# Kernel tuning notes

Hardware: AMD Instinct MI355X
Metric: run time of the kernel (lower is better)

The kernel has to match this reference:

```python
import jax, jax.numpy as jnp
import numpy as np

SIGMA = 1.0
DELTA = 1.0
TOPK = 10
TOPK_HALF = 5  # int(np.around(TOPK / 2))


def l2norm(x):
    # F.normalize: x / max(||x||, 1e-12)
    n = jnp.linalg.norm(x, axis=-1, keepdims=True)
    return x / jnp.maximum(n, 1e-12)


def cdist(a, b):
    # pairwise euclidean distance with grad-safe sqrt (0 on exact-zero dists)
    d2 = (jnp.sum(a * a, axis=1)[:, None] + jnp.sum(b * b, axis=1)[None, :]
          - 2.0 * a @ b.T)
    d2 = jnp.maximum(d2, 0.0)
    return jnp.where(d2 > 0.0, jnp.sqrt(jnp.where(d2 > 0.0, d2, 1.0)), 0.0)


def rc_weights(t_emb, idx):
    # all of this is under torch.no_grad() in the original
    N = t_emb.shape[0]
    T_dist = cdist(t_emb, t_emb)
    W_P = jnp.exp(-(T_dist ** 2) / SIGMA)
    same_id = idx[:, None] == idx[None, :]
    W_P_copy = jnp.where(same_id, 1.0, W_P)
    _, topk_index = jax.lax.top_k(W_P_copy, TOPK)            # [N, k]
    topk_half_index = topk_index[:, :TOPK_HALF]               # [N, k/2]
    rows = jnp.arange(N)[:, None]
    W_NN = jnp.zeros((N, N), W_P.dtype).at[rows, topk_index].set(1.0)
    V = (((W_NN + W_NN.T) / 2.0) == 1.0).astype(W_P.dtype)    # mutual-NN graph
    # vectorized form of the per-row loop:
    # W_C_tilda[i, j] = V[i, j] * |N(i) \cap N(j)| / |N(i)|
    deg = V.sum(axis=1)                                       # |N(i)| per row
    VV = V @ V                                                # V symmetric -> (V@V)[i,j] = |N(i) cap N(j)|
    W_C_tilda = jnp.where(V > 0.0, VV / jnp.maximum(deg, 1.0)[:, None], 0.0)
    W_C_hat = W_C_tilda[topk_half_index].mean(axis=1)         # [N, N]
    W_C = (W_C_hat + W_C_hat.T) / 2.0
    W = (W_P + W_C) / 2.0
    off_diag = 1.0 - jnp.eye(N, dtype=W.dtype)
    pos_weight = W * off_diag
    neg_weight = (1.0 - W) * off_diag
    return pos_weight, neg_weight


def rc_loss(s_emb, t_emb, idx):
    s_emb = l2norm(s_emb)        # disable_mu=True
    t_emb = l2norm(t_emb)
    N = s_emb.shape[0]
    S_dist = cdist(s_emb, s_emb)
    S_dist = S_dist / S_dist.mean(axis=1, keepdims=True)
    pos_w, neg_w = rc_weights(t_emb, idx)
    pos_w = jax.lax.stop_gradient(pos_w)
    neg_w = jax.lax.stop_gradient(neg_w)
    pull = jax.nn.relu(S_dist) ** 2 * pos_w
    push = jax.nn.relu(DELTA - S_dist) ** 2 * neg_w
    return (pull.sum() + push.sum()) / (N * (N - 1))


def kl_loss(s_f, s_g):
    # disable_mu=True -> normalize both
    s_f = l2norm(s_f)
    s_g = l2norm(s_g)
    N = s_f.shape[0]
    S_dist = cdist(s_f, s_f)
    S_dist = S_dist / S_dist.mean(axis=1, keepdims=True)
    S_bg = cdist(s_g, s_g)
    S_bg = S_bg / S_bg.mean(axis=1, keepdims=True)
    log_q = jax.nn.log_softmax(-S_dist, axis=-1)
    log_p = jax.nn.log_softmax(jax.lax.stop_gradient(-S_bg), axis=-1)
    p = jnp.exp(log_p)
    return jnp.sum(p * (log_p - log_q)) / N


def setup_inputs() -> dict:
    key = jax.random.key(0)
    k1, k2, k3, k4 = jax.random.split(key, 4)
    N = 4096
    s_f = jax.random.normal(k1, (N, 512), jnp.float32)
    s_g = jax.random.normal(k2, (N, 512), jnp.float32)
    t_g = jax.random.normal(k3, (N, 1024), jnp.float32)
    idx = jax.random.randint(k4, (N,), 0, 2048, jnp.int64 if jax.config.jax_enable_x64 else jnp.int32)
    return {"s_f": s_f, "s_g": s_g, "t_g": t_g, "idx": idx}


def reference(s_f, s_g, t_g, idx):
    loss_RC_f = rc_loss(s_f, t_g, idx)
    loss_RC_g = rc_loss(s_g, t_g, idx)
    loss_RC = (loss_RC_f + loss_RC_g) / 2.0
    loss_KL = kl_loss(s_f, s_g)
    return loss_RC, loss_KL, loss_RC + loss_KL
```

## Files before the change

kernel.cpp:

```cpp
#include <hip/hip_runtime.h>
#include <hip/hip_bf16.h>

#define NN 4096
typedef unsigned short u16;
typedef __bf16 bf16x8 __attribute__((ext_vector_type(8)));
typedef float f32x4 __attribute__((ext_vector_type(4)));
typedef u16 u16x8 __attribute__((ext_vector_type(8)));

typedef const __attribute__((address_space(1))) void* gptr_t;
typedef __attribute__((address_space(3))) void* lptr_t;

__device__ inline u16 bf16bits(float v) {
    __bf16 h = (__bf16)v;
    return __builtin_bit_cast(u16, h);
}
__device__ inline float bf16val(float v) {
    __bf16 h = (__bf16)v;
    return (float)h;
}
__device__ inline float b2f(u16 b) { return __uint_as_float(((unsigned)b) << 16); }

__device__ inline float block_sum(float v, volatile float* sbuf) {
    int lane = threadIdx.x & 63, wv = threadIdx.x >> 6;
#pragma unroll
    for (int o = 32; o > 0; o >>= 1) v += __shfl_xor(v, o, 64);
    if (lane == 0) sbuf[wv] = v;
    __syncthreads();
    float r = sbuf[0] + sbuf[1] + sbuf[2] + sbuf[3];
    __syncthreads();
    return r;
}

template <int D>
__global__ void normalize_kernel(const float* __restrict__ in, u16* __restrict__ outb,
                                 float* __restrict__ ssout) {
    __shared__ float sbuf[4];
    constexpr int NV = D / 4;
    int row = blockIdx.x, tid = threadIdx.x;
    const float4* x4 = (const float4*)(in + (size_t)row * D);
    float4 v = make_float4(0.f, 0.f, 0.f, 0.f);
    if (tid < NV) v = x4[tid];
    float s = v.x * v.x + v.y * v.y + v.z * v.z + v.w * v.w;
    float tot = block_sum(s, sbuf);
    float inv = 1.0f / fmaxf(sqrtf(tot), 1e-12f);
    float sb = 0.f;
    if (tid < NV) {
        float b0 = bf16val(v.x * inv), b1 = bf16val(v.y * inv);
        float b2 = bf16val(v.z * inv), b3 = bf16val(v.w * inv);
        ushort4 o;
        o.x = bf16bits(v.x * inv);
        o.y = bf16bits(v.y * inv);
        o.z = bf16bits(v.z * inv);
        o.w = bf16bits(v.w * inv);
        ((ushort4*)(outb + (size_t)row * D))[tid] = o;
        sb = b0 * b0 + b1 * b1 + b2 * b2 + b3 * b3;
    }
    float totb = block_sum(sb, sbuf);
    if (tid == 0) ssout[row] = totb;
}

#define TS 132
__launch_bounds__(256)
__global__ void gram_merged(const u16* __restrict__ tb, const u16* __restrict__ fb,
                            const u16* __restrict__ gb, const float* __restrict__ ss_t,
                            const float* __restrict__ ss_f, const float* __restrict__ ss_g,
                            u16* __restrict__ WP, u16* __restrict__ Sf, u16* __restrict__ Sg) {
    __shared__ __align__(16) u16 smem[24576];

    int bid = blockIdx.x;
    int seg = (bid < 528) ? 0 : (bid < 1056 ? 1 : 2);
    int p = bid - seg * 528;
    int l = (p & 7) * 66 + (p >> 3);
    int by = 0, rem = l;
    while (rem >= 32 - by) { rem -= 32 - by; ++by; }
    int bx = by + rem;

    const u16* X = (seg == 0) ? tb : (seg == 1 ? fb : gb);
    const float* ss = (seg == 0) ? ss_t : (seg == 1 ? ss_f : ss_g);
    u16* outp = (seg == 0) ? WP : (seg == 1 ? Sf : Sg);
    const int K = (seg == 0) ? 1024 : 512;
    const bool mode1 = (seg != 0);
    const bool offdiag = (bx != by);

    const int tid = threadIdx.x;
    const int wv = tid >> 6, lane = tid & 63;
    const int wr = wv >> 1, wc = wv & 1;
    const int brow = by * 128, bcol = bx * 128;
    const int r = lane & 15, kc = lane >> 4;
    const int crow = lane >> 2;
    const int koff = (lane & 3) * 8;

    f32x4 acc[4][4];
#pragma unroll
    for (int mi = 0; mi < 4; ++mi)
#pragma unroll
        for (int ni = 0; ni < 4; ++ni) acc[mi][ni] = (f32x4){0.f, 0.f, 0.f, 0.f};

    auto STAGE = [&](int buf, int k0) {
#pragma unroll
        for (int cc = 0; cc < 2; ++cc) {
            int c = wv * 2 + cc;
            const u16* ga = X + (size_t)(brow + c * 16 + crow) * K + k0 + koff;
            const u16* gbp = X + (size_t)(bcol + c * 16 + crow) * K + k0 + koff;
            __builtin_amdgcn_global_load_lds((gptr_t)ga, (lptr_t)&smem[buf * 4096 + c * 512], 16, 0, 0);
            __builtin_amdgcn_global_load_lds((gptr_t)gbp, (lptr_t)&smem[12288 + buf * 4096 + c * 512], 16, 0, 0);
        }
    };

    const int NT = K / 32;
    STAGE(0, 0);
    STAGE(1, 32);
    for (int t = 0; t < NT; ++t) {
        int cur = t % 3;
        if (t == NT - 1) asm volatile("s_waitcnt vmcnt(0)" ::: "memory");
        else             asm volatile("s_waitcnt vmcnt(4)" ::: "memory");
        __builtin_amdgcn_sched_barrier(0);
        __builtin_amdgcn_s_barrier();
        __builtin_amdgcn_sched_barrier(0);

        bf16x8 af[4], bfr[4];
#pragma unroll
        for (int mi = 0; mi < 4; ++mi)
            af[mi] = *(const bf16x8*)&smem[cur * 4096 + (wr * 64 + mi * 16 + r) * 32 + kc * 8];
#pragma unroll
        for (int ni = 0; ni < 4; ++ni)
            bfr[ni] = *(const bf16x8*)&smem[12288 + cur * 4096 + (wc * 64 + ni * 16 + r) * 32 + kc * 8];

        if (t + 2 < NT) STAGE((t + 2) % 3, (t + 2) * 32);

        asm volatile("s_waitcnt lgkmcnt(0)" ::: "memory");
        __builtin_amdgcn_sched_barrier(0);

#pragma unroll
        for (int mi = 0; mi < 4; ++mi)
#pragma unroll
            for (int ni = 0; ni < 4; ++ni)
                acc[mi][ni] = __builtin_amdgcn_mfma_f32_16x16x32_bf16(af[mi], bfr[ni], acc[mi][ni], 0, 0, 0);
    }
    __syncthreads();

    u16* tile = smem;
    const int q = lane >> 4;
#pragma unroll
    for (int mi = 0; mi < 4; ++mi) {
#pragma unroll
        for (int v = 0; v < 4; ++v) {
            int rl = wr * 64 + mi * 16 + q * 4 + v;
            float ssi = ss[brow + rl];
#pragma unroll
            for (int ni = 0; ni < 4; ++ni) {
                int cl = wc * 64 + ni * 16 + r;
                float d2 = fmaxf(ssi + ss[bcol + cl] - 2.0f * acc[mi][ni][v], 0.f);
                float o = mode1 ? sqrtf(d2) : __expf(-d2);
                tile[rl * TS + cl] = bf16bits(o);
            }
        }
    }
    __syncthreads();

    {
        int rl = tid >> 1, hf = tid & 1;
        const u16* srow = &tile[rl * TS + hf * 64];
        u16* drow = outp + (size_t)(brow + rl) * NN + bcol + hf * 64;
#pragma unroll
        for (int i = 0; i < 8; ++i) {
            ushort4 aa = *(const ushort4*)(srow + i * 8);
            ushort4 bb = *(const ushort4*)(srow + i * 8 + 4);
            u16x8 pk = {aa.x, aa.y, aa.z, aa.w, bb.x, bb.y, bb.z, bb.w};
            *(u16x8*)(drow + i * 8) = pk;
        }
    }

    if (offdiag) {
        int c = tid >> 1, hf = tid & 1;
        u16* drow = outp + (size_t)(bcol + c) * NN + brow + hf * 64;
#pragma unroll
        for (int s = 0; s < 8; ++s) {
            u16 g[8];
#pragma unroll
            for (int u = 0; u < 8; ++u) g[u] = tile[(hf * 64 + s * 8 + u) * TS + c];
            u16x8 pk = {g[0], g[1], g[2], g[3], g[4], g[5], g[6], g[7]};
            *(u16x8*)(drow + s * 8) = pk;
        }
    }
}

__global__ void topk_kernel(const u16* __restrict__ WP, const int* __restrict__ idx,
                            int* __restrict__ topk) {
    __shared__ unsigned long long sred[4];
    __shared__ unsigned long long sbest;
    int row = blockIdx.x, tid = threadIdx.x;
    int myid = idx[row];
    const u16x8* W8 = (const u16x8*)(WP + (size_t)row * NN);
    const int4* idx4 = (const int4*)idx;
    unsigned key[16];
#pragma unroll
    for (int a = 0; a < 2; ++a) {
        u16x8 w = W8[a * 256 + tid];
        int4 iA = idx4[a * 512 + tid * 2];
        int4 iB = idx4[a * 512 + tid * 2 + 1];
        int ids[8] = {iA.x, iA.y, iA.z, iA.w, iB.x, iB.y, iB.z, iB.w};
#pragma unroll
        for (int c = 0; c < 8; ++c)
            key[a * 8 + c] = (ids[c] == myid) ? 0x3F800000u : (((unsigned)w[c]) << 16);
    }
    int lane = tid & 63, wv = tid >> 6;
    for (int it = 0; it < 10; ++it) {
        unsigned long long best = 0;
#pragma unroll
        for (int a = 0; a < 2; ++a)
#pragma unroll
            for (int c = 0; c < 8; ++c) {
                unsigned j = (unsigned)(a * 2048 + tid * 8 + c);
                unsigned long long pk =
                    ((unsigned long long)key[a * 8 + c] << 32) | (0xFFFFFFFFu - j);
                if (pk > best) best = pk;
            }
#pragma unroll
        for (int o = 32; o > 0; o >>= 1) {
            unsigned long long t = __shfl_xor(best, o, 64);
            if (t > best) best = t;
        }
        if (lane == 0) sred[wv] = best;
        __syncthreads();
        if (tid == 0) {
            unsigned long long b = sred[0];
            for (int w2 = 1; w2 < 4; ++w2)
                if (sred[w2] > b) b = sred[w2];
            sbest = b;
        }
        __syncthreads();
        unsigned jstar = 0xFFFFFFFFu - (unsigned)(sbest & 0xFFFFFFFFu);
        if (tid == 0) topk[row * 10 + it] = (int)jstar;
        if (((jstar >> 3) & 255u) == (unsigned)tid) {
            unsigned slot = ((jstar >> 11) << 3) | (jstar & 7u);
#pragma unroll
            for (int a = 0; a < 16; ++a)
                if ((unsigned)a == slot) key[a] = 0u;
        }
        __syncthreads();
    }
}

__global__ void mutual_kernel(const int* __restrict__ topk, int* __restrict__ nbr,
                              int* __restrict__ deg) {
    int gid = blockIdx.x * 256 + threadIdx.x;
    if (gid >= NN * 10) return;
    int i = gid / 10, a = gid - i * 10;
    int j = topk[i * 10 + a];
    bool mut = false;
#pragma unroll
    for (int b = 0; b < 10; ++b) mut = mut || (topk[j * 10 + b] == i);
    nbr[gid] = mut ? j : -1;
    if (mut) atomicAdd(&deg[i], 1);
}

__global__ void tilda_kernel(const int* __restrict__ nbr, const int* __restrict__ deg,
                             float* __restrict__ tvals) {
    int gid = blockIdx.x * 256 + threadIdx.x;
    if (gid >= NN * 10) return;
    int m = gid / 10;
    int j = nbr[gid];
    if (j < 0) { tvals[gid] = 0.f; return; }
    int am[10], aj[10];
#pragma unroll
    for (int p = 0; p < 10; ++p) am[p] = nbr[m * 10 + p];
#pragma unroll
    for (int p = 0; p < 10; ++p) aj[p] = nbr[j * 10 + p];
    int cnt = 0;
#pragma unroll
    for (int p = 0; p < 10; ++p)
#pragma unroll
        for (int qq = 0; qq < 10; ++qq)
            cnt += (am[p] >= 0 && am[p] == aj[qq]) ? 1 : 0;
    int dm = deg[m];
    float dv = (float)(dm > 1 ? dm : 1);
    tvals[gid] = (float)cnt / dv;
}

__global__ void hat_kernel(const int* __restrict__ topk, const int* __restrict__ nbr,
                           const float* __restrict__ tvals, int* __restrict__ hcols,
                           float* __restrict__ hvals) {
    int gid = blockIdx.x * 256 + threadIdx.x;
    if (gid >= NN * 5) return;
    int i = gid / 5, h = gid - i * 5;
    int m = topk[i * 10 + h];
#pragma unroll
    for (int a = 0; a < 10; ++a) {
        int j = nbr[m * 10 + a];
        int slot = i * 50 + h * 10 + a;
        hcols[slot] = j;
        hvals[slot] = (j >= 0) ? tvals[m * 10 + a] * 0.2f : 0.f;
    }
}

__global__ void fused_dense_kernel(const u16* __restrict__ Sf, const u16* __restrict__ Sg,
                                   const u16* __restrict__ WP, float* __restrict__ rsf,
                                   float* __restrict__ rsg, double* __restrict__ acc) {
    __shared__ float sbuf[4];
    int row = blockIdx.x, tid = threadIdx.x;
    const u16x8* f8 = (const u16x8*)(Sf + (size_t)row * NN);
    const u16x8* g8 = (const u16x8*)(Sg + (size_t)row * NN);
    const u16x8* w8 = (const u16x8*)(WP + (size_t)row * NN);
    u16x8 fr[2], gr[2];
#pragma unroll
    for (int a = 0; a < 2; ++a) {
        fr[a] = f8[a * 256 + tid];
        gr[a] = g8[a * 256 + tid];
    }
    float sf_ = 0.f, sg_ = 0.f;
#pragma unroll
    for (int a = 0; a < 2; ++a)
#pragma unroll
        for (int c = 0; c < 8; ++c) {
            sf_ += b2f(fr[a][c]);
            sg_ += b2f(gr[a][c]);
        }
    float rsum_f = block_sum(sf_, sbuf);
    float rsum_g = block_sum(sg_, sbuf);
    if (tid == 0) {
        rsf[row] = rsum_f;
        rsg[row] = rsum_g;
    }
    float imf = (float)NN / rsum_f;
    float img = (float)NN / rsum_g;
    float vf[16], vg[16];
#pragma unroll
    for (int a = 0; a < 2; ++a)
#pragma unroll
        for (int c = 0; c < 8; ++c) {
            vf[a * 8 + c] = b2f(fr[a][c]) * imf;
            vg[a * 8 + c] = b2f(gr[a][c]) * img;
        }
    float ef = 0.f, eg = 0.f;
#pragma unroll
    for (int a = 0; a < 16; ++a) {
        ef += __expf(-vf[a]);
        eg += __expf(-vg[a]);
    }
    float lf = logf(block_sum(ef, sbuf));
    float lg = logf(block_sum(eg, sbuf));
    u16x8 wr2[2];
#pragma unroll
    for (int a = 0; a < 2; ++a) wr2[a] = w8[a * 256 + tid];
    float af = 0.f, ag = 0.f, akl = 0.f;
#pragma unroll
    for (int a = 0; a < 2; ++a) {
#pragma unroll
        for (int c = 0; c < 8; ++c) {
            int j = a * 2048 + tid * 8 + c;
            float wp = b2f(wr2[a][c]);
            float sf = vf[a * 8 + c], sg = vg[a * 8 + c];
            if (j != row) {
                float t = fmaxf(1.f - sf, 0.f);
                float pu = t * t;
                float gq = sf * sf - pu;
                af += pu + 0.5f * gq * wp;
                t = fmaxf(1.f - sg, 0.f);
                pu = t * t;
                gq = sg * sg - pu;
                ag += pu + 0.5f * gq * wp;
            }
            float lq = -sf - lf;
            float lp = -sg - lg;
            float pp = __expf(lp);
            akl += pp * (lp - lq);
        }
    }
    float tf = block_sum(af, sbuf);
    float tg2 = block_sum(ag, sbuf);
    float tk = block_sum(akl, sbuf);
    if (tid == 0) {
        int bank = (row & 63) * 8;
        atomicAdd(&acc[bank + 0], (double)tf);
        atomicAdd(&acc[bank + 1], (double)tg2);
        atomicAdd(&acc[bank + 2], (double)tk);
    }
}

__global__ void sparse_kernel(const u16* __restrict__ Sf, const u16* __restrict__ Sg,
                              const int* __restrict__ hcols, const float* __restrict__ hvals,
                              const float* __restrict__ rsf, const float* __restrict__ rsg,
                              double* __restrict__ acc) {
    __shared__ float sbuf[4];
    int lane = threadIdx.x & 63, wv = threadIdx.x >> 6;
    int i = blockIdx.x * 4 + wv;
    float cf = 0.f, cg = 0.f;
    if (lane < 50) {
        int j = hcols[i * 50 + lane];
        if (j >= 0 && j != i) {
            float v = hvals[i * 50 + lane];
            float imfi = (float)NN / rsf[i];
            float imgi = (float)NN / rsg[i];
            float s1 = b2f(Sf[(size_t)i * NN + j]) * imfi;
            float s2 = b2f(Sf[(size_t)j * NN + i]) * ((float)NN / rsf[j]);
            float t1 = fmaxf(1.f - s1, 0.f), t2 = fmaxf(1.f - s2, 0.f);
            cf = v * ((s1 * s1 - t1 * t1) + (s2 * s2 - t2 * t2));
            s1 = b2f(Sg[(size_t)i * NN + j]) * imgi;
            s2 = b2f(Sg[(size_t)j * NN + i]) * ((float)NN / rsg[j]);
            t1 = fmaxf(1.f - s1, 0.f);
            t2 = fmaxf(1.f - s2, 0.f);
            cg = v * ((s1 * s1 - t1 * t1) + (s2 * s2 - t2 * t2));
        }
    }
    float tf = block_sum(cf, sbuf);
    float tg = block_sum(cg, sbuf);
    if (threadIdx.x == 0) {
        int bank = (blockIdx.x & 63) * 8;
        atomicAdd(&acc[bank + 0], (double)(0.25f * tf));
        atomicAdd(&acc[bank + 1], (double)(0.25f * tg));
    }
}

__global__ void finalize_kernel(const double* __restrict__ acc, float* __restrict__ out) {
    if (threadIdx.x == 0) {
        double a0 = 0.0, a1 = 0.0, a2 = 0.0;
        for (int b = 0; b < 64; ++b) {
            a0 += acc[b * 8 + 0];
            a1 += acc[b * 8 + 1];
            a2 += acc[b * 8 + 2];
        }
        double denom = (double)NN * (double)(NN - 1);
        double rcf = a0 / denom, rcg = a1 / denom;
        double rc = 0.5 * (rcf + rcg);
        double kl = a2 / (double)NN;
        out[0] = (float)rc;
        out[1] = (float)kl;
        out[2] = (float)(rc + kl);
    }
}

extern "C" void kernel_launch(void* const* d_in, const int* in_sizes, int n_in, void* d_out,
                              int out_size, void* d_ws, size_t ws_size, hipStream_t stream) {
    const float* s_f = (const float*)d_in[0];
    const float* s_g = (const float*)d_in[1];
    const float* t_g = (const float*)d_in[2];
    const int* idx = (const int*)d_in[3];
    float* out = (float*)d_out;

    char* base = (char*)d_ws;
    size_t off = 0;
    auto alloc = [&](size_t b) {
        char* p = base + off;
        off = (off + b + 255) & ~(size_t)255;
        return p;
    };
    double* acc = (double*)alloc(64 * 8 * 8);
    int* deg = (int*)alloc(NN * 4);
    size_t zero_bytes = off;
    float* rowsum_f = (float*)alloc(NN * 4);
    float* rowsum_g = (float*)alloc(NN * 4);
    u16* tb = (u16*)alloc((size_t)NN * 1024 * 2);
    u16* fb = (u16*)alloc((size_t)NN * 512 * 2);
    u16* gb = (u16*)alloc((size_t)NN * 512 * 2);
    float* ss_t = (float*)alloc(NN * 4);
    float* ss_f = (float*)alloc(NN * 4);
    float* ss_g = (float*)alloc(NN * 4);
    u16* WP = (u16*)alloc((size_t)NN * NN * 2);
    u16* Sf = (u16*)alloc((size_t)NN * NN * 2);
    u16* Sg = (u16*)alloc((size_t)NN * NN * 2);
    int* topk = (int*)alloc(NN * 10 * 4);
    int* nbr = (int*)alloc(NN * 10 * 4);
    float* tvals = (float*)alloc(NN * 10 * 4);
    int* hcols = (int*)alloc(NN * 50 * 4);
    float* hvals = (float*)alloc(NN * 50 * 4);

    hipMemsetAsync(d_ws, 0, zero_bytes, stream);

    normalize_kernel<1024><<<NN, 256, 0, stream>>>(t_g, tb, ss_t);
    normalize_kernel<512><<<NN, 256, 0, stream>>>(s_f, fb, ss_f);
    normalize_kernel<512><<<NN, 256, 0, stream>>>(s_g, gb, ss_g);

    gram_merged<<<1584, 256, 0, stream>>>(tb, fb, gb, ss_t, ss_f, ss_g, WP, Sf, Sg);

    topk_kernel<<<NN, 256, 0, stream>>>(WP, idx, topk);
    mutual_kernel<<<(NN * 10 + 255) / 256, 256, 0, stream>>>(topk, nbr, deg);
    tilda_kernel<<<(NN * 10 + 255) / 256, 256, 0, stream>>>(nbr, deg, tvals);
    hat_kernel<<<(NN * 5 + 255) / 256, 256, 0, stream>>>(topk, nbr, tvals, hcols, hvals);

    fused_dense_kernel<<<NN, 256, 0, stream>>>(Sf, Sg, WP, rowsum_f, rowsum_g, acc);
    sparse_kernel<<<NN / 4, 256, 0, stream>>>(Sf, Sg, hcols, hvals, rowsum_f, rowsum_g, acc);
    finalize_kernel<<<1, 64, 0, stream>>>(acc, out);
}
```

Before: 194.7 us.

## Widen symmetric Gram tiles to 128x256 with a two-pass transposed epilogue

Each Gram block now computes a 128x256 output tile instead of 128x128, so the upper-triangle tile map is rebuilt around 256-wide column blocks. This cuts the grid from 1584 to 816 blocks and lets each A-operand slice feed twice as many MFMAs, reducing LDS and global traffic per output element. The epilogue writes the tile in two 128-column halves, each stored both directly and transposed. The cost is twice the accumulator registers (lower occupancy), more shared memory, and some diagonal-adjacent 128x128 blocks being computed and written by two different workgroups.

```diff
diff --git a/kernel.cpp b/kernel.cpp
--- a/kernel.cpp
+++ b/kernel.cpp
@@ -65,45 +65,48 @@
                             const u16* __restrict__ gb, const float* __restrict__ ss_t,
                             const float* __restrict__ ss_f, const float* __restrict__ ss_g,
                             u16* __restrict__ WP, u16* __restrict__ Sf, u16* __restrict__ Sg) {
-    __shared__ __align__(16) u16 smem[24576];
+    __shared__ __align__(16) u16 smem[36864];
 
     int bid = blockIdx.x;
-    int seg = (bid < 528) ? 0 : (bid < 1056 ? 1 : 2);
-    int p = bid - seg * 528;
-    int l = (p & 7) * 66 + (p >> 3);
-    int by = 0, rem = l;
-    while (rem >= 32 - by) { rem -= 32 - by; ++by; }
-    int bx = by + rem;
+    int seg = (bid < 272) ? 0 : (bid < 544 ? 1 : 2);
+    int p = bid - seg * 272;
+    int l = (p & 7) * 34 + (p >> 3);
+    int ti = 0, rem = l;
+    while (rem >= 16 - (ti >> 1)) { rem -= 16 - (ti >> 1); ++ti; }
+    int c = (ti >> 1) + rem;
 
     const u16* X = (seg == 0) ? tb : (seg == 1 ? fb : gb);
     const float* ss = (seg == 0) ? ss_t : (seg == 1 ? ss_f : ss_g);
     u16* outp = (seg == 0) ? WP : (seg == 1 ? Sf : Sg);
     const int K = (seg == 0) ? 1024 : 512;
     const bool mode1 = (seg != 0);
-    const bool offdiag = (bx != by);
 
     const int tid = threadIdx.x;
     const int wv = tid >> 6, lane = tid & 63;
     const int wr = wv >> 1, wc = wv & 1;
-    const int brow = by * 128, bcol = bx * 128;
+    const int brow = ti * 128, bcol = c * 256;
     const int r = lane & 15, kc = lane >> 4;
     const int crow = lane >> 2;
     const int koff = (lane & 3) * 8;
 
-    f32x4 acc[4][4];
+    f32x4 acc[4][8];
 #pragma unroll
     for (int mi = 0; mi < 4; ++mi)
 #pragma unroll
-        for (int ni = 0; ni < 4; ++ni) acc[mi][ni] = (f32x4){0.f, 0.f, 0.f, 0.f};
+        for (int ni = 0; ni < 8; ++ni) acc[mi][ni] = (f32x4){0.f, 0.f, 0.f, 0.f};
 
     auto STAGE = [&](int buf, int k0) {
 #pragma unroll
         for (int cc = 0; cc < 2; ++cc) {
-            int c = wv * 2 + cc;
-            const u16* ga = X + (size_t)(brow + c * 16 + crow) * K + k0 + koff;
-            const u16* gbp = X + (size_t)(bcol + c * 16 + crow) * K + k0 + koff;
-            __builtin_amdgcn_global_load_lds((gptr_t)ga, (lptr_t)&smem[buf * 4096 + c * 512], 16, 0, 0);
-            __builtin_amdgcn_global_load_lds((gptr_t)gbp, (lptr_t)&smem[12288 + buf * 4096 + c * 512], 16, 0, 0);
+            int c8 = wv * 2 + cc;
+            const u16* ga = X + (size_t)(brow + c8 * 16 + crow) * K + k0 + koff;
+            __builtin_amdgcn_global_load_lds((gptr_t)ga, (lptr_t)&smem[buf * 4096 + c8 * 512], 16, 0, 0);
+        }
+#pragma unroll
+        for (int cc = 0; cc < 4; ++cc) {
+            int c16 = wv * 4 + cc;
+            const u16* gbp = X + (size_t)(bcol + c16 * 16 + crow) * K + k0 + koff;
+            __builtin_amdgcn_global_load_lds((gptr_t)gbp, (lptr_t)&smem[12288 + buf * 8192 + c16 * 512], 16, 0, 0);
         }
     };
 
@@ -113,18 +116,18 @@
     for (int t = 0; t < NT; ++t) {
         int cur = t % 3;
         if (t == NT - 1) asm volatile("s_waitcnt vmcnt(0)" ::: "memory");
-        else             asm volatile("s_waitcnt vmcnt(4)" ::: "memory");
+        else             asm volatile("s_waitcnt vmcnt(6)" ::: "memory");
         __builtin_amdgcn_sched_barrier(0);
         __builtin_amdgcn_s_barrier();
         __builtin_amdgcn_sched_barrier(0);
 
-        bf16x8 af[4], bfr[4];
+        bf16x8 af[4], bfr[8];
 #pragma unroll
         for (int mi = 0; mi < 4; ++mi)
             af[mi] = *(const bf16x8*)&smem[cur * 4096 + (wr * 64 + mi * 16 + r) * 32 + kc * 8];
 #pragma unroll
-        for (int ni = 0; ni < 4; ++ni)
-            bfr[ni] = *(const bf16x8*)&smem[12288 + cur * 4096 + (wc * 64 + ni * 16 + r) * 32 + kc * 8];
+        for (int ni = 0; ni < 8; ++ni)
+            bfr[ni] = *(const bf16x8*)&smem[12288 + cur * 8192 + (wc * 128 + ni * 16 + r) * 32 + kc * 8];
 
         if (t + 2 < NT) STAGE((t + 2) % 3, (t + 2) * 32);
 
@@ -134,7 +137,7 @@
 #pragma unroll
         for (int mi = 0; mi < 4; ++mi)
 #pragma unroll
-            for (int ni = 0; ni < 4; ++ni)
+            for (int ni = 0; ni < 8; ++ni)
                 acc[mi][ni] = __builtin_amdgcn_mfma_f32_16x16x32_bf16(af[mi], bfr[ni], acc[mi][ni], 0, 0, 0);
     }
     __syncthreads();
@@ -142,45 +145,50 @@
     u16* tile = smem;
     const int q = lane >> 4;
 #pragma unroll
-    for (int mi = 0; mi < 4; ++mi) {
-#pragma unroll
-        for (int v = 0; v < 4; ++v) {
-            int rl = wr * 64 + mi * 16 + q * 4 + v;
-            float ssi = ss[brow + rl];
-#pragma unroll
-            for (int ni = 0; ni < 4; ++ni) {
-                int cl = wc * 64 + ni * 16 + r;
-                float d2 = fmaxf(ssi + ss[bcol + cl] - 2.0f * acc[mi][ni][v], 0.f);
-                float o = mode1 ? sqrtf(d2) : __expf(-d2);
-                tile[rl * TS + cl] = bf16bits(o);
+    for (int h = 0; h < 2; ++h) {
+        if (h) __syncthreads();
+        if (wc == h) {
+#pragma unroll
+            for (int mi = 0; mi < 4; ++mi) {
+#pragma unroll
+                for (int v = 0; v < 4; ++v) {
+                    int rl = wr * 64 + mi * 16 + q * 4 + v;
+                    float ssi = ss[brow + rl];
+#pragma unroll
+                    for (int ni = 0; ni < 8; ++ni) {
+                        int cl = ni * 16 + r;
+                        float d2 = fmaxf(ssi + ss[bcol + h * 128 + cl] - 2.0f * acc[mi][ni][v], 0.f);
+                        float o = mode1 ? sqrtf(d2) : __expf(-d2);
+                        tile[rl * TS + cl] = bf16bits(o);
+                    }
+                }
             }
         }
-    }
-    __syncthreads();
-
-    {
-        int rl = tid >> 1, hf = tid & 1;
-        const u16* srow = &tile[rl * TS + hf * 64];
-        u16* drow = outp + (size_t)(brow + rl) * NN + bcol + hf * 64;
-#pragma unroll
-        for (int i = 0; i < 8; ++i) {
-            ushort4 aa = *(const ushort4*)(srow + i * 8);
-            ushort4 bb = *(const ushort4*)(srow + i * 8 + 4);
-            u16x8 pk = {aa.x, aa.y, aa.z, aa.w, bb.x, bb.y, bb.z, bb.w};
-            *(u16x8*)(drow + i * 8) = pk;
-        }
-    }
-
-    if (offdiag) {
-        int c = tid >> 1, hf = tid & 1;
-        u16* drow = outp + (size_t)(bcol + c) * NN + brow + hf * 64;
-#pragma unroll
-        for (int s = 0; s < 8; ++s) {
-            u16 g[8];
-#pragma unroll
-            for (int u = 0; u < 8; ++u) g[u] = tile[(hf * 64 + s * 8 + u) * TS + c];
-            u16x8 pk = {g[0], g[1], g[2], g[3], g[4], g[5], g[6], g[7]};
-            *(u16x8*)(drow + s * 8) = pk;
+        __syncthreads();
+
+        {
+            int rl = tid >> 1, hf = tid & 1;
+            const u16* srow = &tile[rl * TS + hf * 64];
+            u16* drow = outp + (size_t)(brow + rl) * NN + bcol + h * 128 + hf * 64;
+#pragma unroll
+            for (int i = 0; i < 8; ++i) {
+                ushort4 aa = *(const ushort4*)(srow + i * 8);
+                ushort4 bb = *(const ushort4*)(srow + i * 8 + 4);
+                u16x8 pk = {aa.x, aa.y, aa.z, aa.w, bb.x, bb.y, bb.z, bb.w};
+                *(u16x8*)(drow + i * 8) = pk;
+            }
+        }
+        {
+            int c2 = tid >> 1, hf = tid & 1;
+            u16* drow = outp + (size_t)(bcol + h * 128 + c2) * NN + brow + hf * 64;
+#pragma unroll
+            for (int s = 0; s < 8; ++s) {
+                u16 g[8];
+#pragma unroll
+                for (int u = 0; u < 8; ++u) g[u] = tile[(hf * 64 + s * 8 + u) * TS + c2];
+                u16x8 pk = {g[0], g[1], g[2], g[3], g[4], g[5], g[6], g[7]};
+                *(u16x8*)(drow + s * 8) = pk;
+            }
         }
     }
 }
@@ -471,7 +479,7 @@
     normalize_kernel<512><<<NN, 256, 0, stream>>>(s_f, fb, ss_f);
     normalize_kernel<512><<<NN, 256, 0, stream>>>(s_g, gb, ss_g);
 
-    gram_merged<<<1584, 256, 0, stream>>>(tb, fb, gb, ss_t, ss_f, ss_g, WP, Sf, Sg);
+    gram_merged<<<816, 256, 0, stream>>>(tb, fb, gb, ss_t, ss_f, ss_g, WP, Sf, Sg);
 
     topk_kernel<<<NN, 256, 0, stream>>>(WP, idx, topk);
     mutual_kernel<<<(NN * 10 + 255) / 256, 256, 0, stream>>>(topk, nbr, deg);
```

New measurement: 280.2 us. 1.44x slower.

## Compute per-wave top-10 lists independently and merge them once per row

Applied to the files above, without the earlier changes.

The top-k kernel now lets each 64-lane wave pick its own top-10 from its slice without block-wide barriers per iteration. The wave lists are stored in shared memory, and thread 0 merges the four sorted lists after a single barrier. This removes two or three __syncthreads per iteration, leaving one for the whole kernel. Separately, the dense kernel issues the WP row load up front alongside the other loads so its latency overlaps the reductions, at the cost of extra live registers.

```diff
diff --git a/kernel.cpp b/kernel.cpp
--- a/kernel.cpp
+++ b/kernel.cpp
@@ -187,9 +187,9 @@
 
 __global__ void topk_kernel(const u16* __restrict__ WP, const int* __restrict__ idx,
                             int* __restrict__ topk) {
-    __shared__ unsigned long long sred[4];
-    __shared__ unsigned long long sbest;
+    __shared__ unsigned long long wlist[4][10];
     int row = blockIdx.x, tid = threadIdx.x;
+    int lane = tid & 63, wv = tid >> 6;
     int myid = idx[row];
     const u16x8* W8 = (const u16x8*)(WP + (size_t)row * NN);
     const int4* idx4 = (const int4*)idx;
@@ -204,7 +204,6 @@
         for (int c = 0; c < 8; ++c)
             key[a * 8 + c] = (ids[c] == myid) ? 0x3F800000u : (((unsigned)w[c]) << 16);
     }
-    int lane = tid & 63, wv = tid >> 6;
     for (int it = 0; it < 10; ++it) {
         unsigned long long best = 0;
 #pragma unroll
@@ -221,24 +220,30 @@
             unsigned long long t = __shfl_xor(best, o, 64);
             if (t > best) best = t;
         }
-        if (lane == 0) sred[wv] = best;
-        __syncthreads();
-        if (tid == 0) {
-            unsigned long long b = sred[0];
-            for (int w2 = 1; w2 < 4; ++w2)
-                if (sred[w2] > b) b = sred[w2];
-            sbest = b;
-        }
-        __syncthreads();
-        unsigned jstar = 0xFFFFFFFFu - (unsigned)(sbest & 0xFFFFFFFFu);
-        if (tid == 0) topk[row * 10 + it] = (int)jstar;
+        if (lane == 0) wlist[wv][it] = best;
+        unsigned jstar = 0xFFFFFFFFu - (unsigned)(best & 0xFFFFFFFFu);
         if (((jstar >> 3) & 255u) == (unsigned)tid) {
             unsigned slot = ((jstar >> 11) << 3) | (jstar & 7u);
 #pragma unroll
             for (int a = 0; a < 16; ++a)
                 if ((unsigned)a == slot) key[a] = 0u;
         }
-        __syncthreads();
+    }
+    __syncthreads();
+    if (tid == 0) {
+        int h0 = 0, h1 = 0, h2 = 0, h3 = 0;
+        for (int it = 0; it < 10; ++it) {
+            unsigned long long c0 = wlist[0][h0], c1 = wlist[1][h1];
+            unsigned long long c2 = wlist[2][h2], c3 = wlist[3][h3];
+            unsigned long long m01 = c0 > c1 ? c0 : c1;
+            unsigned long long m23 = c2 > c3 ? c2 : c3;
+            unsigned long long m = m01 > m23 ? m01 : m23;
+            if (m == c0) ++h0;
+            else if (m == c1) ++h1;
+            else if (m == c2) ++h2;
+            else ++h3;
+            topk[row * 10 + it] = (int)(0xFFFFFFFFu - (unsigned)(m & 0xFFFFFFFFu));
+        }
     }
 }
 
@@ -302,11 +307,12 @@
     const u16x8* f8 = (const u16x8*)(Sf + (size_t)row * NN);
     const u16x8* g8 = (const u16x8*)(Sg + (size_t)row * NN);
     const u16x8* w8 = (const u16x8*)(WP + (size_t)row * NN);
-    u16x8 fr[2], gr[2];
+    u16x8 fr[2], gr[2], wr2[2];
 #pragma unroll
     for (int a = 0; a < 2; ++a) {
         fr[a] = f8[a * 256 + tid];
         gr[a] = g8[a * 256 + tid];
+        wr2[a] = w8[a * 256 + tid];
     }
     float sf_ = 0.f, sg_ = 0.f;
 #pragma unroll
@@ -340,9 +346,6 @@
     }
     float lf = logf(block_sum(ef, sbuf));
     float lg = logf(block_sum(eg, sbuf));
-    u16x8 wr2[2];
-#pragma unroll
-    for (int a = 0; a < 2; ++a) wr2[a] = w8[a * 256 + tid];
     float af = 0.f, ag = 0.f, akl = 0.f;
 #pragma unroll
     for (int a = 0; a < 2; ++a) {
```

Measured after the change: 197.0 us. About the same (+1.2%).
